# Kernel optimization log

Measured on AMD Instinct MI355X. Metric: run time of the kernel, lower is better.

## Reference

```python
import jax, jax.numpy as jnp
import numpy as np

EPS = 1e-5

def group_norm(x, num_groups, eps=EPS):
    # x: [B, C, H, W]; no affine (matches F.group_norm with weight=None)
    B, C, H, W = x.shape
    xg = x.reshape(B, num_groups, (C // num_groups) * H * W)
    mean = jnp.mean(xg, axis=-1, keepdims=True)
    var = jnp.var(xg, axis=-1, keepdims=True)
    xg = (xg - mean) * jax.lax.rsqrt(var + eps)
    return xg.reshape(B, C, H, W)

def setup_inputs() -> dict:
    key = jax.random.key(0)
    ks = jax.random.split(key, 5)
    B, C, H, W = 32, 256, 32, 32
    # kaiming-uniform-ish scale for linear weights
    bound = 1.0 / np.sqrt(C)
    x = jax.random.normal(ks[0], (B, C, H, W), dtype=jnp.float32)
    WQ = jax.random.uniform(ks[1], (C, C), jnp.float32, -bound, bound)
    WK = jax.random.uniform(ks[2], (C, C), jnp.float32, -bound, bound)
    WV = jax.random.uniform(ks[3], (C, C), jnp.float32, -bound, bound)
    Wo = jax.random.uniform(ks[4], (C, C), jnp.float32, -bound, bound)
    z = jnp.zeros((C,), jnp.float32)
    return {"x": x, "WQ": WQ, "bQ": z, "WK": WK, "bK": z,
            "WV": WV, "bV": z, "Wo": Wo, "bo": z}

def reference(x, WQ, bQ, WK, bK, WV, bV, Wo, bo):
    B, C, H, W = x.shape
    G = min(32, C)
    h = group_norm(x, G)                      # [B,C,H,W]
    h = h.reshape(B, C, H * W).transpose(0, 2, 1)  # [B, S, C], S = H*W
    q = h @ WQ + bQ
    k = h @ WK + bK
    v = h @ WV + bV
    scale = C ** (-0.5)
    attn = jnp.einsum('bsc,btc->bst', q, k) * scale   # [B,S,S]
    attn = jax.nn.softmax(attn, axis=-1)
    o = jnp.einsum('bst,btc->bsc', attn, v)           # [B,S,C]
    o = o @ Wo + bo                                   # output Nin while in [B,S,C]
    o = o.transpose(0, 2, 1).reshape(B, C, H, W)
    return x + o
```

## Files before the change

kernel.cpp:

```cpp
#include <hip/hip_runtime.h>
#include <stdint.h>

#define BB  32
#define CC  256
#define SS  1024
#define GG  32
#define GCH 8
#define EPS 1e-5f

typedef __attribute__((ext_vector_type(8))) short short8;
typedef __attribute__((ext_vector_type(4))) float f32x4;
typedef __attribute__((ext_vector_type(16))) float f32x16;
typedef unsigned short ushort;

__device__ __forceinline__ float bf2f(ushort u){
  union { unsigned int i; float f; } v; v.i = ((unsigned int)u) << 16; return v.f;
}
__device__ __forceinline__ ushort f2bf(float f){
  union { float f; unsigned int i; } v; v.f = f;
  unsigned int r = v.i + 0x7FFFu + ((v.i >> 16) & 1u);
  return (ushort)(r >> 16);
}
__device__ __forceinline__ unsigned int cvt_pk_bf16(float lo, float hi){
  unsigned int r;
  asm("v_cvt_pk_bf16_f32 %0, %1, %2" : "=v"(r) : "v"(lo), "v"(hi));
  return r;
}

typedef __attribute__((address_space(3))) unsigned int lds_uint;
typedef const __attribute__((address_space(1))) unsigned int glob_uint;
__device__ __forceinline__ void ld_lds16(const void* g, void* l){
  __builtin_amdgcn_global_load_lds((glob_uint*)g, (lds_uint*)l, 16, 0, 0);
}

__global__ __launch_bounds__(256) void sniff_k(const unsigned int* __restrict__ xw,
                                               int* __restrict__ flag)
{
  const int tid = threadIdx.x;
  unsigned int w = xw[tid];
  ushort lo = (ushort)(w & 0xFFFFu);
  int e = (lo >> 7) & 0xFF;
  int ok = (lo == 0 || (e >= 100 && e <= 130)) ? 1 : 0;
  __shared__ int cnt;
  if (tid == 0) cnt = 0;
  __syncthreads();
  atomicAdd(&cnt, ok);
  __syncthreads();
  if (tid == 0) *flag = (cnt > 192) ? 1 : 0;
}

__global__ __launch_bounds__(256) void convert_pre(
    const void* w0, const void* w1, const void* w2, const void* w3,
    const void* b0, const void* b1, const void* b2, const void* b3,
    ushort* __restrict__ WT, float* __restrict__ biasF,
    const int* __restrict__ flag)
{
  const int f = *flag;
  const int z = blockIdx.z;
  const float scl = (z == 0) ? 0.0901684400557f : 1.0f;
  const void* wsel = z==0?w0:z==1?w1:z==2?w2:w3;
  ushort* dst = WT + (long long)z * 65536;
  __shared__ ushort t[64][65];
  const int tid = threadIdx.x;
  const int tx = tid & 63, ty = tid >> 6;
  const int r0 = blockIdx.x * 64, c0 = blockIdx.y * 64;
  for (int j = 0; j < 64; j += 4){
    const int idx = (r0+ty+j)*256 + c0+tx;
    float v = f ? bf2f(((const ushort*)wsel)[idx]) : ((const float*)wsel)[idx];
    t[ty+j][tx] = f2bf(v * scl);
  }
  __syncthreads();
  for (int j = 0; j < 64; j += 4) dst[(c0+ty+j)*256 + r0+tx] = t[tx][ty+j];
  if (blockIdx.x == 0 && blockIdx.y == 0){
    const void* bsel = z==0?b0:z==1?b1:z==2?b2:b3;
    float bv = f ? bf2f(((const ushort*)bsel)[tid]) : ((const float*)bsel)[tid];
    biasF[z*256 + tid] = bv * scl;
  }
}

__global__ __launch_bounds__(256) void gn_stats(const void* __restrict__ x,
                                                float* __restrict__ stats,
                                                const int* __restrict__ flag)
{
  const int f = *flag;
  const int g = blockIdx.x, b = blockIdx.y;
  const int tid = threadIdx.x;
  const long long base = ((long long)b * CC + g * GCH) * SS;
  float sum = 0.f, ss = 0.f;
  if (f){
    const ushort* xg = (const ushort*)x + base;
    #pragma unroll
    for (int j = 0; j < 4; j++){
      uint4 u = *(const uint4*)(xg + (j*256 + tid)*8);
      const ushort* e = (const ushort*)&u;
      #pragma unroll
      for (int i = 0; i < 8; i++){ float v = bf2f(e[i]); sum += v; ss += v*v; }
    }
  } else {
    const float* xg = (const float*)x + base;
    #pragma unroll
    for (int j = 0; j < 8; j++){
      float4 v4 = *(const float4*)(xg + (j*256 + tid)*4);
      sum += v4.x+v4.y+v4.z+v4.w;
      ss  += v4.x*v4.x+v4.y*v4.y+v4.z*v4.z+v4.w*v4.w;
    }
  }
  __shared__ float red[8];
  const int lane = tid & 63, w = tid >> 6;
  #pragma unroll
  for (int o = 32; o > 0; o >>= 1){
    sum += __shfl_down(sum, o);
    ss  += __shfl_down(ss, o);
  }
  if (lane == 0){ red[w] = sum; red[4+w] = ss; }
  __syncthreads();
  if (tid == 0){
    float s1 = red[0]+red[1]+red[2]+red[3];
    float s2 = red[4]+red[5]+red[6]+red[7];
    float mean = s1 / (float)(GCH*SS);
    float var  = s2 / (float)(GCH*SS) - mean*mean;
    const int idx = b*GG + g;
    stats[idx*2]   = mean;
    stats[idx*2+1] = rsqrtf(var + EPS);
  }
}

__global__ __launch_bounds__(256) void gn_norm(const void* __restrict__ x,
                                               ushort* __restrict__ h,
                                               const float* __restrict__ stats,
                                               const int* __restrict__ flag)
{
  const int f = *flag;
  const int c0 = blockIdx.x * 64, s0 = blockIdx.y * 64, b = blockIdx.z;
  const int tid = threadIdx.x;
  __shared__ ushort T[64][72];
  const int row = tid >> 2;
  const int qr  = tid & 3;
  const int g = (c0 + row) >> 3;
  const float mean = stats[(b*GG + g)*2];
  const float rstd = stats[(b*GG + g)*2 + 1];
  const long long xrow = ((long long)b * CC + c0 + row) * SS + s0;
  if (f){
    const ushort* xr = (const ushort*)x + xrow;
    #pragma unroll
    for (int j = 0; j < 2; j++){
      const int col = qr*16 + j*8;
      uint4 u = *(const uint4*)(xr + col);
      const ushort* e = (const ushort*)&u;
      #pragma unroll
      for (int i = 0; i < 8; i++) T[row][col+i] = f2bf((bf2f(e[i]) - mean) * rstd);
    }
  } else {
    const float* xr = (const float*)x + xrow;
    #pragma unroll
    for (int j = 0; j < 4; j++){
      const int col = qr*16 + j*4;
      float4 v4 = *(const float4*)(xr + col);
      T[row][col+0] = f2bf((v4.x - mean) * rstd);
      T[row][col+1] = f2bf((v4.y - mean) * rstd);
      T[row][col+2] = f2bf((v4.z - mean) * rstd);
      T[row][col+3] = f2bf((v4.w - mean) * rstd);
    }
  }
  __syncthreads();
  #pragma unroll
  for (int pass = 0; pass < 2; pass++){
    const int sr = pass*32 + (tid >> 3);
    const int cl = (tid & 7) * 8;
    ushort tmp[8];
    #pragma unroll
    for (int e = 0; e < 8; e++) tmp[e] = T[cl+e][sr];
    *(uint4*)(&h[((long long)b * SS + s0 + sr) * CC + c0 + cl]) = *(const uint4*)tmp;
  }
}

template<int MODE>
__global__ __launch_bounds__(256) void gemm128(
    const ushort* __restrict__ A,
    const ushort* __restrict__ BT,
    ushort* __restrict__ Cmat,
    int lda, int ldb, int ldc, int K,
    long long sA, long long sB, long long sC,
    const float* __restrict__ biasF,
    const void* __restrict__ xres,
    void* __restrict__ outp,
    ushort* __restrict__ vTp,
    long long xoff,
    const int* __restrict__ flag)
{
  extern __shared__ __attribute__((aligned(16))) ushort smem[];
  ushort* As = smem;
  ushort* Bs = smem + 8192;
  const int tid  = threadIdx.x;
  const int lane = tid & 63;
  const int w    = tid >> 6;
  const int wr   = w >> 1, wc = w & 1;
  const int bz   = blockIdx.z;
  const int m0 = blockIdx.x * 128;
  const int n0 = blockIdx.y * 128;

  const int rr = lane & 15;
  const int hi = lane >> 4;
  const int crow = lane >> 3;
  const int pslot = lane & 7;

  f32x4 acc[4][4] = {};

  const ushort* Ab = A + (long long)bz * sA;
  const ushort* Bb = BT + (long long)bz * sB;

  for (int k0 = 0; k0 < K; k0 += 64){
    #pragma unroll
    for (int j = 0; j < 4; j++){
      const int ck = w*4 + j;
      const int r  = ck*8 + crow;
      const int s  = pslot ^ (r & 7);
      ld_lds16(Ab + (long long)(m0 + r) * lda + k0 + s*8, &As[ck * 512]);
    }
    #pragma unroll
    for (int j = 0; j < 4; j++){
      const int ck = w*4 + j;
      const int r  = ck*8 + crow;
      const int s  = pslot ^ (r & 7);
      ld_lds16(Bb + (long long)(n0 + r) * ldb + k0 + s*8, &Bs[ck * 512]);
    }
    asm volatile("s_waitcnt vmcnt(0)" ::: "memory");
    __builtin_amdgcn_sched_barrier(0);
    __syncthreads();

    #pragma unroll
    for (int kk = 0; kk < 2; kk++){
      short8 af[4], bfr[4];
      const int lbyte = kk*64 + hi*16;
      #pragma unroll
      for (int mf = 0; mf < 4; mf++){
        const int row = wr*64 + mf*16 + rr;
        af[mf] = *(const short8*)((const char*)As + row*128 + (lbyte ^ ((row & 7) << 4)));
      }
      #pragma unroll
      for (int nf = 0; nf < 4; nf++){
        const int row = wc*64 + nf*16 + rr;
        bfr[nf] = *(const short8*)((const char*)Bs + row*128 + (lbyte ^ ((row & 7) << 4)));
      }
      #pragma unroll
      for (int mf = 0; mf < 4; mf++)
        #pragma unroll
        for (int nf = 0; nf < 4; nf++)
          acc[mf][nf] = __builtin_amdgcn_mfma_f32_16x16x32_bf16(af[mf], bfr[nf], acc[mf][nf], 0, 0, 0);
    }
    __syncthreads();
  }

  const int rb = 4 * (lane >> 4);
  if (MODE == 0){
    if (bz < 2){
      ushort* Co = Cmat + (long long)bz * sC;
      #pragma unroll
      for (int mf = 0; mf < 4; mf++){
        #pragma unroll
        for (int nf = 0; nf < 4; nf++){
          const int col = n0 + wc*64 + nf*16 + rr;
          const float badd = biasF[bz*256 + col];
          #pragma unroll
          for (int r = 0; r < 4; r++){
            const int row = m0 + wr*64 + mf*16 + rb + r;
            Co[(long long)row * ldc + col] = f2bf(acc[mf][nf][r] + badd);
          }
        }
      }
    } else {
      #pragma unroll
      for (int mf = 0; mf < 4; mf++){
        #pragma unroll
        for (int nf = 0; nf < 4; nf++){
          const int col = n0 + wc*64 + nf*16 + rr;
          const float badd = biasF[512 + col];
          #pragma unroll
          for (int r = 0; r < 4; r++){
            const int row = m0 + wr*64 + mf*16 + rb + r;
            const int bL = row >> 10, s = row & 1023;
            vTp[((long long)bL * CC + col) * SS + s] = f2bf(acc[mf][nf][r] + badd);
          }
        }
      }
    }
  } else {
    const int bL = m0 >> 10;
    const int s0 = m0 & 1023;
    #pragma unroll
    for (int mf = 0; mf < 4; mf++){
      #pragma unroll
      for (int nf = 0; nf < 4; nf++){
        const int colL = wc*64 + nf*16 + rr;
        const float badd = biasF[768 + n0 + colL];
        #pragma unroll
        for (int r = 0; r < 4; r++){
          const int rowL = wr*64 + mf*16 + rb + r;
          smem[colL * 128 + rowL] = f2bf(acc[mf][nf][r] + badd);
        }
      }
    }
    __syncthreads();
    const int f = *flag;
    for (int i = tid; i < 2048; i += 256){
      const int colL = i >> 4;
      const int rowL = (i & 15) * 8;
      const long long oi = xoff + ((long long)bL * CC + n0 + colL) * SS + s0 + rowL;
      const ushort* pu = &smem[colL * 128 + rowL];
      if (f){
        const ushort* xu = (const ushort*)xres + oi;
        ushort* ou = (ushort*)outp + oi;
        ushort tmp[8];
        #pragma unroll
        for (int e = 0; e < 8; e++) tmp[e] = f2bf(bf2f(xu[e]) + bf2f(pu[e]));
        *(uint4*)ou = *(const uint4*)tmp;
      } else {
        const float* xf = (const float*)xres + oi;
        float* of = (float*)outp + oi;
        float4 a0 = *(const float4*)xf;
        float4 a1 = *(const float4*)(xf + 4);
        float4 r0, r1;
        r0.x = a0.x + bf2f(pu[0]); r0.y = a0.y + bf2f(pu[1]);
        r0.z = a0.z + bf2f(pu[2]); r0.w = a0.w + bf2f(pu[3]);
        r1.x = a1.x + bf2f(pu[4]); r1.y = a1.y + bf2f(pu[5]);
        r1.z = a1.z + bf2f(pu[6]); r1.w = a1.w + bf2f(pu[7]);
        *(float4*)of = r0;
        *(float4*)(of + 4) = r1;
      }
    }
  }
}

__global__ __launch_bounds__(512, 1) void attn_fused(
    const ushort* __restrict__ q, const ushort* __restrict__ k,
    const ushort* __restrict__ vT, ushort* __restrict__ oC)
{
  __shared__ ushort Kb[2][64 * 256];
  __shared__ ushort Vb[2][256 * 64];
  __shared__ float  Mb[8][32];
  __shared__ float  Lb[8][32];
  const int tid = threadIdx.x, lane = tid & 63, w = tid >> 6;
  const int l31 = lane & 31, hi2 = lane >> 5;
  const int qg = w & 3, ch = w >> 2;
  const int b = blockIdx.x, qt = blockIdx.y;

  const char* kgB = (const char*)(k + (long long)b * SS * CC);
  const char* vgB = (const char*)(vT + (long long)b * CC * SS);
  const int qrow = qt*128 + qg*32 + l31;
  const ushort* qgp = q + ((long long)b * SS + qrow) * CC + hi2*8;
  ushort* ogq = oC + ((long long)b * SS + qrow) * CC;

  short8 qf[16];
  #pragma unroll
  for (int kk = 0; kk < 16; kk++)
    qf[kk] = *(const short8*)(qgp + kk*16);

  f32x16 Oa[8] = {};
  float mrow = -1e30f, lrow = 0.0f;

  #define STAGE(buf, t0)                                                        \
  {                                                                             \
    _Pragma("unroll")                                                           \
    for (int j = 0; j < 4; j++){                                                \
      const int ck = j*8 + w;                                                   \
      const int tr = ck*2 + (lane >> 5);                                        \
      const int xb = ((lane & 31) * 16) ^ ((tr & 31) << 4);                     \
      ld_lds16(kgB + (long long)((t0) + tr) * 512 + xb, &Kb[buf][ck * 512]);    \
    }                                                                           \
    _Pragma("unroll")                                                           \
    for (int j = 0; j < 4; j++){                                                \
      const int ck = j*8 + w;                                                   \
      const int vr = ck*2 + (lane >> 5);                                        \
      const int u  = (lane & 31) ^ ((vr & 7) << 2);                             \
      const int vc = vr*4 + (u & 3);                                            \
      const int tb = (u >> 2) * 16;                                             \
      ld_lds16(vgB + (long long)vc * 2048 + (t0)*2 + tb, &Vb[buf][ck * 512]);   \
    }                                                                           \
  }

  STAGE(0, 0);
  asm volatile("s_waitcnt vmcnt(0)" ::: "memory");
  __builtin_amdgcn_sched_barrier(0);
  __syncthreads();

  const int coff = hi2 * 16;
  const int kswz = l31 << 4;
  const int krow = ch*32 + l31;

  for (int t = 0; t < 16; t++){
    const int cur = t & 1;
    if (t < 15) STAGE(cur ^ 1, (t+1)*64);

    f32x16 Sa = {};
    __builtin_amdgcn_s_setprio(1);
    #pragma unroll
    for (int kk = 0; kk < 16; kk++){
      const int off = kk*32 + coff;
      short8 ka = *(const short8*)((const char*)&Kb[cur][0] + krow*512 + (off ^ kswz));
      Sa = __builtin_amdgcn_mfma_f32_32x32x16_bf16(ka, qf[kk], Sa, 0, 0, 0);
    }
    __builtin_amdgcn_s_setprio(0);

    float mx = Sa[0];
    #pragma unroll
    for (int r = 1; r < 16; r++) mx = fmaxf(mx, Sa[r]);
    mx = fmaxf(mx, __shfl_xor(mx, 32));
    if (!__all(mx <= mrow + 8.0f)){
      const float mn = fmaxf(mrow, mx);
      const float sc = __builtin_amdgcn_exp2f(mrow - mn);
      mrow = mn;
      lrow *= sc;
      #pragma unroll
      for (int nf = 0; nf < 8; nf++)
        #pragma unroll
        for (int r = 0; r < 16; r++) Oa[nf][r] *= sc;
    }
    float rs = 0.0f;
    #pragma unroll
    for (int r = 0; r < 16; r++){
      Sa[r] = __builtin_amdgcn_exp2f(Sa[r] - mrow); rs += Sa[r];
    }
    rs += __shfl_xor(rs, 32);
    lrow += rs;

    __builtin_amdgcn_s_setprio(1);
    #pragma unroll
    for (int g = 0; g < 2; g++){
      unsigned int b0 = cvt_pk_bf16(Sa[g*8+0], Sa[g*8+1]);
      unsigned int b1 = cvt_pk_bf16(Sa[g*8+2], Sa[g*8+3]);
      unsigned int b2 = cvt_pk_bf16(Sa[g*8+4], Sa[g*8+5]);
      unsigned int b3 = cvt_pk_bf16(Sa[g*8+6], Sa[g*8+7]);
      unsigned int s0 = (unsigned int)__shfl_xor((int)b0, 32);
      unsigned int s1 = (unsigned int)__shfl_xor((int)b1, 32);
      unsigned int s2 = (unsigned int)__shfl_xor((int)b2, 32);
      unsigned int s3 = (unsigned int)__shfl_xor((int)b3, 32);
      union { uint4 u; short8 s; } pw;
      pw.u.x = hi2 ? s2 : b0;
      pw.u.y = hi2 ? s3 : b1;
      pw.u.z = hi2 ? b2 : s0;
      pw.u.w = hi2 ? b3 : s1;
      const short8 pb = pw.s;
      const int G = ch*4 + g*2 + hi2;
      #pragma unroll
      for (int nf = 0; nf < 8; nf++){
        const int c = nf*32 + l31;
        const int vr = c >> 2;
        const int slot = (((G << 2) | (c & 3)) ^ ((vr & 7) << 2));
        short8 va = *(const short8*)((const char*)&Vb[cur][0] + vr*512 + slot*16);
        Oa[nf] = __builtin_amdgcn_mfma_f32_32x32x16_bf16(va, pb, Oa[nf], 0, 0, 0);
      }
    }
    __builtin_amdgcn_s_setprio(0);

    asm volatile("s_waitcnt vmcnt(0)" ::: "memory");
    __builtin_amdgcn_sched_barrier(0);
    __syncthreads();
  }
  #undef STAGE

  float* Ob = (qg < 2) ? (float*)&Kb[qg][0] : (float*)&Vb[qg - 2][0];
  if (ch == 1){
    #pragma unroll
    for (int nf = 0; nf < 8; nf++){
      #pragma unroll
      for (int r = 0; r < 16; r++){
        const int c = nf*32 + (r & 3) + 8*(r >> 2) + 4*hi2;
        Ob[c*32 + l31] = Oa[nf][r];
      }
    }
    if (hi2 == 0){ Mb[w][l31] = mrow; Lb[w][l31] = lrow; }
  }
  __syncthreads();
  if (ch == 0){
    const float m2 = Mb[w + 4][l31], l2 = Lb[w + 4][l31];
    const float mx = fmaxf(mrow, m2);
    const float f1 = __builtin_amdgcn_exp2f(mrow - mx);
    const float f2 = __builtin_amdgcn_exp2f(m2 - mx);
    const float inv = 1.0f / (f1*lrow + f2*l2);
    const float a1 = f1 * inv, a2 = f2 * inv;
    #pragma unroll
    for (int nf = 0; nf < 8; nf++){
      #pragma unroll
      for (int g = 0; g < 4; g++){
        float o0 = Oa[nf][g*4+0]*a1 + Ob[(nf*32 + g*8 + hi2*4 + 0)*32 + l31]*a2;
        float o1 = Oa[nf][g*4+1]*a1 + Ob[(nf*32 + g*8 + hi2*4 + 1)*32 + l31]*a2;
        float o2 = Oa[nf][g*4+2]*a1 + Ob[(nf*32 + g*8 + hi2*4 + 2)*32 + l31]*a2;
        float o3 = Oa[nf][g*4+3]*a1 + Ob[(nf*32 + g*8 + hi2*4 + 3)*32 + l31]*a2;
        uint2 ov;
        ov.x = cvt_pk_bf16(o0, o1);
        ov.y = cvt_pk_bf16(o2, o3);
        *(uint2*)(ogq + nf*32 + g*8 + hi2*4) = ov;
      }
    }
  }
}

extern "C" void kernel_launch(void* const* d_in, const int* in_sizes, int n_in,
                              void* d_out, int out_size, void* d_ws, size_t ws_size,
                              hipStream_t stream)
{
  (void)in_sizes; (void)n_in; (void)out_size;
  const void* x  = d_in[0];
  const void* WQ = d_in[1];
  const void* bQ = d_in[2];
  const void* WK = d_in[3];
  const void* bK = d_in[4];
  const void* WV = d_in[5];
  const void* bV = d_in[6];
  const void* Wo = d_in[7];
  const void* bo = d_in[8];

  const long long NE  = (long long)BB * SS * CC;
  const long long SC  = (long long)SS * CC;

  uint8_t* base = (uint8_t*)d_ws;
  int* flag          = (int*)base;
  float* biasF       = (float*)(base + 256);
  float* stats       = (float*)(base + 256 + 4096);
  ushort* WT         = (ushort*)(base + 256 + 4096 + 8192);
  ushort* h          = WT + 4 * 65536;

  const long long fixedB = 256 + 4096 + 8192 + 4LL*65536*2 + NE*2;
  int CB = 1;
  for (int c = 32; c >= 1; c >>= 1){
    if (fixedB + 4LL * c * SC * 2 <= (long long)ws_size){ CB = c; break; }
  }

  ushort* q  = h + NE;
  ushort* k  = q + (long long)CB * SC;
  ushort* vT = k + (long long)CB * SC;
  ushort* oC = vT + (long long)CB * SC;

  dim3 blk(256);
  const size_t shmem = 32768;

  sniff_k<<<1, blk, 0, stream>>>((const unsigned int*)x, flag);
  convert_pre<<<dim3(4, 4, 4), blk, 0, stream>>>(WQ, WK, WV, Wo, bQ, bK, bV, bo, WT, biasF, flag);
  gn_stats<<<dim3(GG, BB), blk, 0, stream>>>(x, stats, flag);
  gn_norm<<<dim3(4, 16, BB), blk, 0, stream>>>(x, h, stats, flag);

  for (int c0 = 0; c0 < BB; c0 += CB){
    const ushort* hC = h + (long long)c0 * SC;
    gemm128<0><<<dim3(CB*8, 2, 3), blk, shmem, stream>>>(
        hC, WT, q, CC, CC, CC, CC,
        0LL, 65536LL, (long long)CB * SC,
        biasF, nullptr, nullptr, vT, 0LL, flag);
    attn_fused<<<dim3(CB, 8), dim3(512), 0, stream>>>(q, k, vT, oC);
    gemm128<3><<<dim3(CB*8, 2, 1), blk, shmem, stream>>>(
        oC, WT + 3*65536, nullptr, CC, CC, SS, CC,
        0LL, 0LL, 0LL,
        biasF, x, d_out, nullptr, (long long)c0 * SC, flag);
  }
}
```

Baseline: 140.7 us.

## Inline dtype sniff, stage V transpose through LDS, split QK accumulator chains

Removes the separate single-block sniff kernel and has each kernel detect the input dtype itself from the first words of x, which drops one launch and its serialization. The V-projection epilogue now writes its transposed tile into shared memory and then stores coalesced 16-byte rows instead of scattered 2-byte writes. The QK^T MFMA loop uses two independent accumulators summed afterward to shorten the dependency chain. The cost is redundant sniff loads in every block and extra LDS traffic plus a barrier in the V epilogue.

Result: slower. 153.1 us (+8.8%).

```diff
diff --git a/kernel.cpp b/kernel.cpp
--- a/kernel.cpp
+++ b/kernel.cpp
@@ -27,35 +27,36 @@
   return r;
 }
 
+__device__ __forceinline__ int sniff_inline(const void* xp){
+  const unsigned int* xw = (const unsigned int*)xp;
+  const int lane = threadIdx.x & 63;
+  int ok = 0;
+  #pragma unroll
+  for (int j = 0; j < 4; j++){
+    unsigned int w = xw[lane*4 + j];
+    ushort lo = (ushort)(w & 0xFFFFu);
+    int e = (lo >> 7) & 0xFF;
+    ok += (lo == 0 || (e >= 100 && e <= 130)) ? 1 : 0;
+  }
+  #pragma unroll
+  for (int o = 32; o > 0; o >>= 1) ok += __shfl_down(ok, o);
+  ok = __shfl(ok, 0);
+  return ok > 192;
+}
+
 typedef __attribute__((address_space(3))) unsigned int lds_uint;
 typedef const __attribute__((address_space(1))) unsigned int glob_uint;
 __device__ __forceinline__ void ld_lds16(const void* g, void* l){
   __builtin_amdgcn_global_load_lds((glob_uint*)g, (lds_uint*)l, 16, 0, 0);
 }
 
-__global__ __launch_bounds__(256) void sniff_k(const unsigned int* __restrict__ xw,
-                                               int* __restrict__ flag)
-{
-  const int tid = threadIdx.x;
-  unsigned int w = xw[tid];
-  ushort lo = (ushort)(w & 0xFFFFu);
-  int e = (lo >> 7) & 0xFF;
-  int ok = (lo == 0 || (e >= 100 && e <= 130)) ? 1 : 0;
-  __shared__ int cnt;
-  if (tid == 0) cnt = 0;
-  __syncthreads();
-  atomicAdd(&cnt, ok);
-  __syncthreads();
-  if (tid == 0) *flag = (cnt > 192) ? 1 : 0;
-}
-
 __global__ __launch_bounds__(256) void convert_pre(
+    const void* x,
     const void* w0, const void* w1, const void* w2, const void* w3,
     const void* b0, const void* b1, const void* b2, const void* b3,
-    ushort* __restrict__ WT, float* __restrict__ biasF,
-    const int* __restrict__ flag)
+    ushort* __restrict__ WT, float* __restrict__ biasF)
 {
-  const int f = *flag;
+  const int f = sniff_inline(x);
   const int z = blockIdx.z;
   const float scl = (z == 0) ? 0.0901684400557f : 1.0f;
   const void* wsel = z==0?w0:z==1?w1:z==2?w2:w3;
@@ -79,10 +80,9 @@
 }
 
 __global__ __launch_bounds__(256) void gn_stats(const void* __restrict__ x,
-                                                float* __restrict__ stats,
-                                                const int* __restrict__ flag)
+                                                float* __restrict__ stats)
 {
-  const int f = *flag;
+  const int f = sniff_inline(x);
   const int g = blockIdx.x, b = blockIdx.y;
   const int tid = threadIdx.x;
   const long long base = ((long long)b * CC + g * GCH) * SS;
@@ -127,10 +127,9 @@
 
 __global__ __launch_bounds__(256) void gn_norm(const void* __restrict__ x,
                                                ushort* __restrict__ h,
-                                               const float* __restrict__ stats,
-                                               const int* __restrict__ flag)
+                                               const float* __restrict__ stats)
 {
-  const int f = *flag;
+  const int f = sniff_inline(x);
   const int c0 = blockIdx.x * 64, s0 = blockIdx.y * 64, b = blockIdx.z;
   const int tid = threadIdx.x;
   __shared__ ushort T[64][72];
@@ -185,8 +184,7 @@
     const void* __restrict__ xres,
     void* __restrict__ outp,
     ushort* __restrict__ vTp,
-    long long xoff,
-    const int* __restrict__ flag)
+    long long xoff)
 {
   extern __shared__ __attribute__((aligned(16))) ushort smem[];
   ushort* As = smem;
@@ -273,15 +271,23 @@
       for (int mf = 0; mf < 4; mf++){
         #pragma unroll
         for (int nf = 0; nf < 4; nf++){
-          const int col = n0 + wc*64 + nf*16 + rr;
-          const float badd = biasF[512 + col];
+          const int colL = wc*64 + nf*16 + rr;
+          const float badd = biasF[512 + n0 + colL];
           #pragma unroll
           for (int r = 0; r < 4; r++){
-            const int row = m0 + wr*64 + mf*16 + rb + r;
-            const int bL = row >> 10, s = row & 1023;
-            vTp[((long long)bL * CC + col) * SS + s] = f2bf(acc[mf][nf][r] + badd);
+            const int rowL = wr*64 + mf*16 + rb + r;
+            smem[colL * 128 + rowL] = f2bf(acc[mf][nf][r] + badd);
           }
         }
+      }
+      __syncthreads();
+      const int bL = m0 >> 10;
+      const int s0 = m0 & 1023;
+      for (int i = tid; i < 2048; i += 256){
+        const int colL = i >> 4;
+        const int rowL = (i & 15) * 8;
+        uint4 pv = *(const uint4*)(&smem[colL * 128 + rowL]);
+        *(uint4*)(&vTp[((long long)bL * CC + n0 + colL) * SS + s0 + rowL]) = pv;
       }
     }
   } else {
@@ -301,7 +307,7 @@
       }
     }
     __syncthreads();
-    const int f = *flag;
+    const int f = sniff_inline(xres);
     for (int i = tid; i < 2048; i += 256){
       const int colL = i >> 4;
       const int rowL = (i & 15) * 8;
@@ -391,15 +397,21 @@
     const int cur = t & 1;
     if (t < 15) STAGE(cur ^ 1, (t+1)*64);
 
-    f32x16 Sa = {};
+    f32x16 SaE = {}, SaO = {};
     __builtin_amdgcn_s_setprio(1);
     #pragma unroll
-    for (int kk = 0; kk < 16; kk++){
-      const int off = kk*32 + coff;
-      short8 ka = *(const short8*)((const char*)&Kb[cur][0] + krow*512 + (off ^ kswz));
-      Sa = __builtin_amdgcn_mfma_f32_32x32x16_bf16(ka, qf[kk], Sa, 0, 0, 0);
+    for (int kk = 0; kk < 16; kk += 2){
+      const int off0 = kk*32 + coff;
+      const int off1 = (kk+1)*32 + coff;
+      short8 ka0 = *(const short8*)((const char*)&Kb[cur][0] + krow*512 + (off0 ^ kswz));
+      short8 ka1 = *(const short8*)((const char*)&Kb[cur][0] + krow*512 + (off1 ^ kswz));
+      SaE = __builtin_amdgcn_mfma_f32_32x32x16_bf16(ka0, qf[kk],   SaE, 0, 0, 0);
+      SaO = __builtin_amdgcn_mfma_f32_32x32x16_bf16(ka1, qf[kk+1], SaO, 0, 0, 0);
     }
     __builtin_amdgcn_s_setprio(0);
+    f32x16 Sa;
+    #pragma unroll
+    for (int r = 0; r < 16; r++) Sa[r] = SaE[r] + SaO[r];
 
     float mx = Sa[0];
     #pragma unroll
@@ -514,7 +526,6 @@
   const long long SC  = (long long)SS * CC;
 
   uint8_t* base = (uint8_t*)d_ws;
-  int* flag          = (int*)base;
   float* biasF       = (float*)(base + 256);
   float* stats       = (float*)(base + 256 + 4096);
   ushort* WT         = (ushort*)(base + 256 + 4096 + 8192);
@@ -534,21 +545,20 @@
   dim3 blk(256);
   const size_t shmem = 32768;
 
-  sniff_k<<<1, blk, 0, stream>>>((const unsigned int*)x, flag);
-  convert_pre<<<dim3(4, 4, 4), blk, 0, stream>>>(WQ, WK, WV, Wo, bQ, bK, bV, bo, WT, biasF, flag);
-  gn_stats<<<dim3(GG, BB), blk, 0, stream>>>(x, stats, flag);
-  gn_norm<<<dim3(4, 16, BB), blk, 0, stream>>>(x, h, stats, flag);
+  convert_pre<<<dim3(4, 4, 4), blk, 0, stream>>>(x, WQ, WK, WV, Wo, bQ, bK, bV, bo, WT, biasF);
+  gn_stats<<<dim3(GG, BB), blk, 0, stream>>>(x, stats);
+  gn_norm<<<dim3(4, 16, BB), blk, 0, stream>>>(x, h, stats);
 
   for (int c0 = 0; c0 < BB; c0 += CB){
     const ushort* hC = h + (long long)c0 * SC;
     gemm128<0><<<dim3(CB*8, 2, 3), blk, shmem, stream>>>(
         hC, WT, q, CC, CC, CC, CC,
         0LL, 65536LL, (long long)CB * SC,
-        biasF, nullptr, nullptr, vT, 0LL, flag);
+        biasF, nullptr, nullptr, vT, 0LL);
     attn_fused<<<dim3(CB, 8), dim3(512), 0, stream>>>(q, k, vT, oC);
     gemm128<3><<<dim3(CB*8, 2, 1), blk, shmem, stream>>>(
         oC, WT + 3*65536, nullptr, CC, CC, SS, CC,
         0LL, 0LL, 0LL,
-        biasF, x, d_out, nullptr, (long long)c0 * SC, flag);
-  }
-}
+        biasF, x, d_out, nullptr, (long long)c0 * SC);
+  }
+}
```
